# Optimization experiments

Hardware: AMD Instinct MI355X
Metric: run time of the kernel (lower is better)

Reference implementation:

```python
import jax, jax.numpy as jnp
import numpy as np
from jax import lax

B, E, D, N, R, K = 4, 768, 1536, 16, 48, 4
H, W = 16, 16
L = H * W
NDIR = 4


def _perms():
    idx = np.arange(L)
    idx_v = np.arange(L).reshape(H, W).T.reshape(-1)  # column-major (vertical) scan order
    perms = [idx, idx[::-1].copy(), idx_v, idx_v[::-1].copy()]
    invs = [np.argsort(p) for p in perms]
    return [jnp.asarray(p) for p in perms], [jnp.asarray(p) for p in invs]

PERMS, INVS = _perms()


def setup_inputs() -> dict:
    key = jax.random.key(0)
    ks = jax.random.split(key, 10)
    hidden_states = jax.random.normal(ks[0], (B, L, E), jnp.float32)
    in_proj_w = jax.random.normal(ks[1], (2 * D, E), jnp.float32) * 0.02
    out_proj_w = jax.random.normal(ks[2], (E, D), jnp.float32) * 0.02
    conv_w = jax.random.normal(ks[3], (NDIR, D, K), jnp.float32) * 0.1
    conv_b = jax.random.normal(ks[4], (NDIR, D), jnp.float32) * 0.1
    xproj_w = jax.random.normal(ks[5], (NDIR, R + 2 * N, D), jnp.float32) * 0.02
    dt_init_std = R ** -0.5
    dtproj_w = jax.random.uniform(ks[6], (NDIR, D, R), jnp.float32, -dt_init_std, dt_init_std)
    dt = jnp.exp(jax.random.uniform(ks[7], (NDIR, D), jnp.float32)
                 * (np.log(0.1) - np.log(0.001)) + np.log(0.001))
    dt = jnp.clip(dt, 1e-4, None)
    dtproj_b = dt + jnp.log(-jnp.expm1(-dt))  # inverse-softplus init as in the module
    A_log = jnp.broadcast_to(
        jnp.log(jnp.arange(1, N + 1, dtype=jnp.float32))[None, None, :], (NDIR, D, N)).copy()
    D_param = jnp.ones((NDIR, D), jnp.float32)
    return dict(hidden_states=hidden_states, in_proj_w=in_proj_w, out_proj_w=out_proj_w,
                conv_w=conv_w, conv_b=conv_b, xproj_w=xproj_w, dtproj_w=dtproj_w,
                dtproj_b=dtproj_b, A_log=A_log, D_param=D_param)


def _mamba_dir(xz, cw, cb, xw, dtw, dtb, a_log, dpar):
    # xz: (B, 2D, L) in this direction's scan order
    x, z = xz[:, :D], xz[:, D:]
    # causal depthwise conv1d + SiLU (mamba_inner_fn conv path)
    x = lax.conv_general_dilated(x, cw[:, None, :], (1,), [(K - 1, 0)],
                                 feature_group_count=D,
                                 dimension_numbers=('NCH', 'OIH', 'NCH'))
    x = jax.nn.silu(x + cb[None, :, None])
    # x_proj -> dt, B, C
    x_dbl = jnp.einsum('bdl,kd->bkl', x, xw)
    dt, Bm, Cm = x_dbl[:, :R], x_dbl[:, R:R + N], x_dbl[:, R + N:]
    delta = jax.nn.softplus(jnp.einsum('brl,dr->bdl', dt, dtw) + dtb[None, :, None])
    A = -jnp.exp(a_log)                                  # (D, N)
    dA = jnp.exp(jnp.einsum('bdl,dn->lbdn', delta, A))   # (L, B, D, N)
    dBu = jnp.einsum('bdl,bnl,bdl->lbdn', delta, Bm, x)  # delta * B * u

    def step(h, inp):
        da, dbu = inp
        h = da * h + dbu
        return h, h

    h0 = jnp.zeros((x.shape[0], D, N), x.dtype)
    _, hs = lax.scan(step, h0, (dA, dBu))                # (L, B, D, N)
    y = jnp.einsum('lbdn,bnl->bdl', hs, Cm) + dpar[None, :, None] * x
    return y * jax.nn.silu(z)                            # gate, (B, D, L)


def reference(hidden_states, in_proj_w, out_proj_w, conv_w, conv_b,
              xproj_w, dtproj_w, dtproj_b, A_log, D_param):
    xz = jnp.einsum('ble,fe->bfl', hidden_states, in_proj_w)  # (B, 2D, L)
    out = jnp.zeros((hidden_states.shape[0], D, L), hidden_states.dtype)
    for i in range(NDIR):  # fixed small set of structurally distinct scan directions
        xz_i = xz[:, :, PERMS[i]]
        y = _mamba_dir(xz_i, conv_w[i], conv_b[i], xproj_w[i], dtproj_w[i],
                       dtproj_b[i], A_log[i], D_param[i])
        out = out + y[:, :, INVS[i]]  # multi_reverse then sum-fusion
    return jnp.einsum('bdl,ed->ble', out, out_proj_w)
```

## Files before the change

### kernel.cpp

```cpp
#include <hip/hip_runtime.h>
#include <hip/hip_bf16.h>

#define BI   4
#define LI   256
#define EI   768
#define DI   1536
#define NI   16
#define RI   48
#define KI   4
#define NDIRS 4
#define F2D  3072
#define MROWS 1024
#define LOG2E 1.4426950408889634f

typedef float    floatx2 __attribute__((ext_vector_type(2)));
typedef float    floatx4 __attribute__((ext_vector_type(4)));
typedef _Float16 halfx2  __attribute__((ext_vector_type(2)));
typedef _Float16 halfx4  __attribute__((ext_vector_type(4)));
typedef _Float16 halfx8  __attribute__((ext_vector_type(8)));

typedef __attribute__((address_space(3))) unsigned lds_u32;
typedef __attribute__((address_space(1))) const unsigned glb_u32;

__device__ __forceinline__ void load16(const _Float16* g, _Float16* l) {
    __builtin_amdgcn_global_load_lds((glb_u32*)g, (lds_u32*)l, 16, 0, 0);
}

__device__ __forceinline__ int perm_idx(int dir, int j) {
    switch (dir) {
        case 0:  return j;
        case 1:  return 255 - j;
        case 2:  return ((j & 15) << 4) | (j >> 4);
        default: return 255 - (((j & 15) << 4) | (j >> 4));
    }
}

template<int CTRL>
__device__ __forceinline__ float dpp_add(float p) {
    int t = __builtin_amdgcn_update_dpp(0, __builtin_bit_cast(int, p),
                                        CTRL, 0xf, 0xf, true);
    return p + __builtin_bit_cast(float, t);
}
__device__ __forceinline__ float grp8_sum(float p) {
    p = dpp_add<0xB1>(p);
    p = dpp_add<0x4E>(p);
    p = dpp_add<0x141>(p);
    return p;
}

template<int BM, int BN, int WGN, int FM, int FN>
__device__ __forceinline__ void gemm_core(const _Float16* __restrict__ Ah,
                                          const _Float16* __restrict__ Al, int lda,
                                          const _Float16* __restrict__ Bh,
                                          const _Float16* __restrict__ Bl, int ldb,
                                          int nChunks, _Float16* smem,
                                          floatx4 (&acc)[FM][FN]) {
    const int tid = threadIdx.x, lane = tid & 63, wave = tid >> 6;
    const int wave_m = wave / WGN, wave_n = wave % WGN;
    _Float16* sAh = smem;
    _Float16* sAl = smem + BM * 32;
    _Float16* sBh = smem + BM * 64;
    _Float16* sBl = smem + BM * 64 + BN * 32;
    const int rr = lane & 15, koff = (lane >> 4) * 8;
    const int arow = wave_m * FM * 16, brow = wave_n * FN * 16;

    for (int c = 0; c < nChunks; ++c) {
        for (int idx = tid; idx < BM * 4; idx += 256) {
            int r = idx >> 2, s = (idx & 3) * 8;
            load16(Ah + (size_t)r * lda + c * 32 + s, sAh + idx * 8);
            load16(Al + (size_t)r * lda + c * 32 + s, sAl + idx * 8);
        }
        for (int idx = tid; idx < BN * 4; idx += 256) {
            int r = idx >> 2, s = (idx & 3) * 8;
            load16(Bh + (size_t)r * ldb + c * 32 + s, sBh + idx * 8);
            load16(Bl + (size_t)r * ldb + c * 32 + s, sBl + idx * 8);
        }
        asm volatile("s_waitcnt vmcnt(0)" ::: "memory");
        __syncthreads();

        halfx8 ahf[FM], alf[FM], bhf[FN], blf[FN];
        #pragma unroll
        for (int i = 0; i < FM; ++i) {
            ahf[i] = *(const halfx8*)(sAh + (arow + i * 16 + rr) * 32 + koff);
            alf[i] = *(const halfx8*)(sAl + (arow + i * 16 + rr) * 32 + koff);
        }
        #pragma unroll
        for (int j = 0; j < FN; ++j) {
            bhf[j] = *(const halfx8*)(sBh + (brow + j * 16 + rr) * 32 + koff);
            blf[j] = *(const halfx8*)(sBl + (brow + j * 16 + rr) * 32 + koff);
        }
        #pragma unroll
        for (int i = 0; i < FM; ++i)
            #pragma unroll
            for (int j = 0; j < FN; ++j) {
                acc[i][j] = __builtin_amdgcn_mfma_f32_16x16x32_f16(ahf[i], bhf[j], acc[i][j], 0, 0, 0);
                acc[i][j] = __builtin_amdgcn_mfma_f32_16x16x32_f16(ahf[i], blf[j], acc[i][j], 0, 0, 0);
                acc[i][j] = __builtin_amdgcn_mfma_f32_16x16x32_f16(alf[i], bhf[j], acc[i][j], 0, 0, 0);
            }
        __syncthreads();
    }
}

__global__ __launch_bounds__(256) void k_splitall(
        const float* __restrict__ hs,  const float* __restrict__ wip,
        const float* __restrict__ wop, const float* __restrict__ xw,
        const float* __restrict__ dtw,
        _Float16* __restrict__ hsh,  _Float16* __restrict__ hsl,
        _Float16* __restrict__ wiph, _Float16* __restrict__ wipl,
        _Float16* __restrict__ woph, _Float16* __restrict__ wopl,
        _Float16* __restrict__ xwh,  _Float16* __restrict__ xwl,
        _Float16* __restrict__ dtwh, _Float16* __restrict__ dtwl) {
    int i4 = (blockIdx.x * 256 + threadIdx.x) * 4;
    floatx4 v;
    _Float16 *dh, *dl; int off;
    if (i4 < 786432)        { off = i4;           v = *(const floatx4*)(hs + off);  dh = hsh;  dl = hsl;  }
    else if (i4 < 3145728)  { off = i4 - 786432;  v = *(const floatx4*)(wip + off); dh = wiph; dl = wipl; }
    else if (i4 < 4325376)  { off = i4 - 3145728; v = *(const floatx4*)(wop + off); dh = woph; dl = wopl; }
    else if (i4 < 4816896)  { off = i4 - 4325376; v = *(const floatx4*)(xw + off);  dh = xwh;  dl = xwl;  }
    else {
        int t0 = i4 - 4816896;
        int col = t0 & 63, dr = t0 >> 6;
        floatx4 z = {0.f, 0.f, 0.f, 0.f};
        v = (col < 48) ? *(const floatx4*)(dtw + (size_t)dr * 48 + col) : z;
        dh = dtwh; dl = dtwl; off = t0;
    }
    halfx4 hh, hl;
    #pragma unroll
    for (int e = 0; e < 4; ++e) {
        _Float16 h = (_Float16)v[e];
        hh[e] = h; hl[e] = (_Float16)(v[e] - (float)h);
    }
    *(halfx4*)(dh + off) = hh;
    *(halfx4*)(dl + off) = hl;
}

__global__ __launch_bounds__(256) void k_inproj_t(const _Float16* __restrict__ Ah,
                                                  const _Float16* __restrict__ Al,
                                                  const _Float16* __restrict__ Bh,
                                                  const _Float16* __restrict__ Bl,
                                                  float* __restrict__ C) {
    __shared__ _Float16 smem[128 * 64 + 128 * 64];
    int row0 = blockIdx.x * 128, col0 = blockIdx.y * 128, k0 = blockIdx.z * 384;
    float* Cp = C + (size_t)blockIdx.z * MROWS * F2D;
    floatx4 acc[4][4] = {};
    gemm_core<128, 128, 2, 4, 4>(Ah + (size_t)row0 * EI + k0, Al + (size_t)row0 * EI + k0, EI,
                                 Bh + (size_t)col0 * EI + k0, Bl + (size_t)col0 * EI + k0, EI,
                                 12, smem, acc);
    int lane = threadIdx.x & 63, wave = threadIdx.x >> 6;
    int cc = lane & 15, q = lane >> 4;
    int rbase = row0 + (wave >> 1) * 64, cbase = col0 + (wave & 1) * 64;
    #pragma unroll
    for (int i = 0; i < 4; ++i)
        #pragma unroll
        for (int j = 0; j < 4; ++j)
            #pragma unroll
            for (int r = 0; r < 4; ++r)
                Cp[(size_t)(rbase + i * 16 + q * 4 + r) * F2D + cbase + j * 16 + cc] = acc[i][j][r];
}

__global__ __launch_bounds__(256) void k_outproj_t(const _Float16* __restrict__ Ah,
                                                   const _Float16* __restrict__ Al,
                                                   const _Float16* __restrict__ Bh,
                                                   const _Float16* __restrict__ Bl,
                                                   float* __restrict__ C) {
    __shared__ _Float16 smem[192 * 64];
    int row0 = blockIdx.x * 64, col0 = blockIdx.y * 128, k0 = blockIdx.z * 384;
    float* Cp = C + (size_t)blockIdx.z * MROWS * EI;
    floatx4 acc[2][4] = {};
    gemm_core<64, 128, 2, 2, 4>(Ah + (size_t)row0 * DI + k0, Al + (size_t)row0 * DI + k0, DI,
                                Bh + (size_t)col0 * DI + k0, Bl + (size_t)col0 * DI + k0, DI,
                                12, smem, acc);
    int lane = threadIdx.x & 63, wave = threadIdx.x >> 6;
    int cc = lane & 15, q = lane >> 4;
    int rbase = row0 + (wave >> 1) * 32, cbase = col0 + (wave & 1) * 64;
    #pragma unroll
    for (int i = 0; i < 2; ++i)
        #pragma unroll
        for (int j = 0; j < 4; ++j)
            #pragma unroll
            for (int r = 0; r < 4; ++r)
                Cp[(size_t)(rbase + i * 16 + q * 4 + r) * EI + cbase + j * 16 + cc] = acc[i][j][r];
}

__global__ __launch_bounds__(256) void k_osum(const float* __restrict__ oacc,
                                              float* __restrict__ out) {
    int i4 = (blockIdx.x * 256 + threadIdx.x) * 4;
    const size_t S = (size_t)MROWS * EI;
    floatx4 s = *(const floatx4*)(oacc + i4) + *(const floatx4*)(oacc + S + i4) +
                *(const floatx4*)(oacc + 2 * S + i4) + *(const floatx4*)(oacc + 3 * S + i4);
    *(floatx4*)(out + i4) = s;
}

__global__ __launch_bounds__(256) void k_xdbl_t(const _Float16* __restrict__ xh,
                                                const _Float16* __restrict__ xl,
                                                const _Float16* __restrict__ xwh,
                                                const _Float16* __restrict__ xwl,
                                                float* __restrict__ C) {
    __shared__ _Float16 smem[208 * 64];
    int row0 = blockIdx.x * 128, dir = blockIdx.y, k0 = blockIdx.z * 192;
    float* Cp = C + (size_t)blockIdx.z * NDIRS * MROWS * 80;
    floatx4 acc[2][5] = {};
    const size_t abase = ((size_t)dir * MROWS + row0) * DI + k0;
    const size_t bbase = (size_t)dir * 80 * DI + k0;
    gemm_core<128, 80, 1, 2, 5>(xh + abase, xl + abase, DI,
                                xwh + bbase, xwl + bbase, DI, 6, smem, acc);
    int lane = threadIdx.x & 63, wave = threadIdx.x >> 6;
    int cc = lane & 15, q = lane >> 4;
    int rbase = row0 + wave * 32;
    #pragma unroll
    for (int i = 0; i < 2; ++i)
        #pragma unroll
        for (int j = 0; j < 5; ++j)
            #pragma unroll
            for (int r = 0; r < 4; ++r)
                Cp[((size_t)dir * MROWS + rbase + i * 16 + q * 4 + r) * 80 + j * 16 + cc] = acc[i][j][r];
}

__global__ __launch_bounds__(256) void k_xsplit(const float* __restrict__ acc,
                                                _Float16* __restrict__ dtqh,
                                                _Float16* __restrict__ dtql,
                                                float* __restrict__ BCm) {
    const size_t PS = (size_t)NDIRS * MROWS * 80;
    int idx = blockIdx.x * 256 + threadIdx.x;
    int dir = idx / (MROWS * 96);
    int rem = idx - dir * MROWS * 96;
    int row = rem / 96, col = rem - row * 96;
    size_t rbase = (size_t)dir * MROWS + row;
    auto sum8 = [&](int c) {
        size_t o = rbase * 80 + c;
        float s = 0.f;
        #pragma unroll
        for (int kp = 0; kp < 8; ++kp) s += acc[kp * PS + o];
        return s;
    };
    if (col < 64) {
        float v = (col < 48) ? sum8(col) : 0.f;
        _Float16 h = (_Float16)v;
        dtqh[rbase * 64 + col] = h;
        dtql[rbase * 64 + col] = (_Float16)(v - (float)h);
    } else if (col < 80) {
        int n = col - 64;
        BCm[rbase * 32 + n * 2] = sum8(48 + n);
    } else {
        int n = col - 80;
        BCm[rbase * 32 + n * 2 + 1] = sum8(64 + n);
    }
}

__global__ __launch_bounds__(256) void k_delta_t(const _Float16* __restrict__ dtqh,
                                                 const _Float16* __restrict__ dtql,
                                                 const _Float16* __restrict__ dtwh,
                                                 const _Float16* __restrict__ dtwl,
                                                 const float* __restrict__ dtb,
                                                 float* __restrict__ delta) {
    __shared__ _Float16 smem[192 * 64];
    int row0 = blockIdx.x * 64, col0 = blockIdx.y * 128, dir = blockIdx.z;
    floatx4 acc[2][4] = {};
    const size_t abase = ((size_t)dir * MROWS + row0) * 64;
    const size_t bbase = ((size_t)dir * DI + col0) * 64;
    gemm_core<64, 128, 2, 2, 4>(dtqh + abase, dtql + abase, 64,
                                dtwh + bbase, dtwl + bbase, 64, 2, smem, acc);
    int lane = threadIdx.x & 63, wave = threadIdx.x >> 6;
    int cc = lane & 15, q = lane >> 4;
    int rbase = row0 + (wave >> 1) * 32, cbase = col0 + (wave & 1) * 64;
    #pragma unroll
    for (int i = 0; i < 2; ++i)
        #pragma unroll
        for (int j = 0; j < 4; ++j) {
            int col = cbase + j * 16 + cc;
            float bias = dtb[(size_t)dir * DI + col];
            #pragma unroll
            for (int r = 0; r < 4; ++r) {
                float v = acc[i][j][r] + bias;
                float sp = (v > 20.f) ? v : log1pf(__expf(v));
                delta[((size_t)dir * MROWS + rbase + i * 16 + q * 4 + r) * DI + col] = sp;
            }
        }
}

__global__ __launch_bounds__(256) void k_conv(const float* __restrict__ xz,
                                              const float* __restrict__ cw,
                                              const float* __restrict__ cb,
                                              _Float16* __restrict__ xh,
                                              _Float16* __restrict__ xl) {
    const size_t S = (size_t)MROWS * F2D;
    int dir = blockIdx.z, b = blockIdx.y;
    int lchunk = blockIdx.x / 6, dsub = blockIdx.x % 6;
    int d = dsub * 256 + threadIdx.x;
    int base = lchunk * 16;

    const float* w = cw + ((size_t)dir * DI + d) * KI;
    float w0 = w[0], w1 = w[1], w2 = w[2], w3 = w[3];
    float bias = cb[(size_t)dir * DI + d];

    auto ld = [&](int m) -> float {
        if (m < 0) return 0.f;
        int src = perm_idx(dir, m);
        size_t o = ((size_t)b * 256 + src) * F2D + d;
        return xz[o] + xz[S + o];
    };
    float xm3 = ld(base - 3), xm2 = ld(base - 2), xm1 = ld(base - 1);

    #pragma unroll
    for (int j = 0; j < 16; ++j) {
        float cur = ld(base + j);
        float s = bias + w0 * xm3 + w1 * xm2 + w2 * xm1 + w3 * cur;
        xm3 = xm2; xm2 = xm1; xm1 = cur;
        float x = s / (1.f + __expf(-s));
        _Float16 h = (_Float16)x;
        size_t o = ((size_t)dir * MROWS + b * 256 + base + j) * DI + d;
        xh[o] = h;
        xl[o] = (_Float16)(x - (float)h);
    }
}

__global__ __launch_bounds__(256) void k_scan(const float* __restrict__ delta,
                                              const _Float16* __restrict__ xhg,
                                              const _Float16* __restrict__ xlg,
                                              const float* __restrict__ BCm,
                                              const float* __restrict__ A_log,
                                              const float* __restrict__ Dp,
                                              float* __restrict__ ydir) {
    const int dchunk = blockIdx.x, b = blockIdx.y, dir = blockIdx.z;
    const int tid = threadIdx.x;
    const int dslot = tid >> 3;
    const int np = tid & 7;
    const int d0 = dchunk * 32, d = d0 + dslot;

    __shared__ float sdx[2][32][64];
    __shared__ float sbc[2][32][32];
    __shared__ float sY[32][32];

    const float Av0 = -__expf(A_log[((size_t)dir * DI + d) * NI + 2 * np]) * LOG2E;
    const float Av1 = -__expf(A_log[((size_t)dir * DI + d) * NI + 2 * np + 1]) * LOG2E;
    const float Dpar = Dp[(size_t)dir * DI + d];
    float h0 = 0.f, h1 = 0.f;

    const size_t dirrow = (size_t)dir * MROWS;
    const int srow = tid >> 3, sc4 = (tid & 7) * 4;

    floatx4 rdel, rbc;
    halfx4 rxh, rxl;
    auto load_chunk = [&](int j0) {
        int row = b * 256 + j0 + srow;
        size_t o = (dirrow + row) * DI + d0 + sc4;
        rdel = *(const floatx4*)(delta + o);
        rxh  = *(const halfx4*)(xhg + o);
        rxl  = *(const halfx4*)(xlg + o);
        rbc  = *(const floatx4*)(BCm + (dirrow + row) * 32 + sc4);
    };

    load_chunk(0);

    for (int c = 0; c < 8; ++c) {
        const int buf = c & 1;
        #pragma unroll
        for (int e = 0; e < 4; ++e) {
            sdx[buf][srow][(sc4 + e) * 2]     = rdel[e];
            sdx[buf][srow][(sc4 + e) * 2 + 1] = (float)rxh[e] + (float)rxl[e];
        }
        *(floatx4*)&sbc[buf][srow][sc4] = rbc;
        __syncthreads();
        if (c < 7) load_chunk((c + 1) * 32);

        #pragma unroll
        for (int jj = 0; jj < 32; ++jj) {
            floatx2 dx = *(const floatx2*)&sdx[buf][jj][dslot * 2];
            floatx4 bc = *(const floatx4*)&sbc[buf][jj][np * 4];
            float dv = dx[0], xv = dx[1];
            float a0 = __builtin_amdgcn_exp2f(dv * Av0);
            float a1 = __builtin_amdgcn_exp2f(dv * Av1);
            float du = dv * xv;
            h0 = fmaf(a0, h0, du * bc[0]);
            h1 = fmaf(a1, h1, du * bc[2]);
            float p = fmaf(h1, bc[3], h0 * bc[1]);
            p = grp8_sum(p);
            if (np == 0) sY[jj][dslot] = fmaf(Dpar, xv, p);
        }
        __syncthreads();

        {
            int lout = perm_idx(dir, c * 32 + srow);
            floatx4 o = *(const floatx4*)&sY[srow][sc4];
            *(floatx4*)&ydir[(dirrow + (size_t)b * 256 + lout) * DI + d0 + sc4] = o;
        }
    }
}

__global__ __launch_bounds__(256) void k_sum(const float* __restrict__ ydir,
                                             const float* __restrict__ xz,
                                             _Float16* __restrict__ yh,
                                             _Float16* __restrict__ yl) {
    int i4 = (blockIdx.x * 256 + threadIdx.x) * 4;
    const size_t S = (size_t)MROWS * DI;
    const size_t SZ = (size_t)MROWS * F2D;
    int row = i4 / DI, dcol = i4 - row * DI;
    size_t zo = (size_t)row * F2D + DI + dcol;
    floatx4 zv = *(const floatx4*)(xz + zo) + *(const floatx4*)(xz + SZ + zo);
    floatx4 s = *(const floatx4*)(ydir + i4) + *(const floatx4*)(ydir + S + i4) +
                *(const floatx4*)(ydir + 2 * S + i4) + *(const floatx4*)(ydir + 3 * S + i4);
    halfx4 hh, hl;
    #pragma unroll
    for (int e = 0; e < 4; ++e) {
        float g = zv[e] / (1.f + __expf(-zv[e]));
        float v = s[e] * g;
        _Float16 h = (_Float16)v;
        hh[e] = h; hl[e] = (_Float16)(v - (float)h);
    }
    *(halfx4*)(yh + i4) = hh;
    *(halfx4*)(yl + i4) = hl;
}

extern "C" void kernel_launch(void* const* d_in, const int* in_sizes, int n_in,
                              void* d_out, int out_size, void* d_ws, size_t ws_size,
                              hipStream_t stream) {
    const float* hs   = (const float*)d_in[0];
    const float* wip  = (const float*)d_in[1];
    const float* wop  = (const float*)d_in[2];
    const float* cw   = (const float*)d_in[3];
    const float* cb   = (const float*)d_in[4];
    const float* xw   = (const float*)d_in[5];
    const float* dtw  = (const float*)d_in[6];
    const float* dtb  = (const float*)d_in[7];
    const float* alog = (const float*)d_in[8];
    const float* dpar = (const float*)d_in[9];
    float* out = (float*)d_out;

    char* p = (char*)d_ws;
    auto alloc_f32 = [&](size_t n) { float* r = (float*)p; p += n * 4; return r; };
    auto alloc_f16 = [&](size_t n) { _Float16* r = (_Float16*)p; p += n * 2; return r; };

    _Float16* hsh  = alloc_f16(786432);
    _Float16* hsl  = alloc_f16(786432);
    _Float16* wiph = alloc_f16(2359296);
    _Float16* wipl = alloc_f16(2359296);
    _Float16* woph = alloc_f16(1179648);
    _Float16* wopl = alloc_f16(1179648);
    _Float16* xwh  = alloc_f16(491520);
    _Float16* xwl  = alloc_f16(491520);
    _Float16* dtwh = alloc_f16((size_t)NDIRS * DI * 64);
    _Float16* dtwl = alloc_f16((size_t)NDIRS * DI * 64);
    float*    xz   = alloc_f32((size_t)2 * MROWS * F2D);
    _Float16* xh   = alloc_f16((size_t)NDIRS * MROWS * DI);
    _Float16* xl   = alloc_f16((size_t)NDIRS * MROWS * DI);
    _Float16* dtqh = alloc_f16((size_t)NDIRS * MROWS * 64);
    _Float16* dtql = alloc_f16((size_t)NDIRS * MROWS * 64);
    float*    BCm  = alloc_f32((size_t)NDIRS * MROWS * 32);
    float*    delta= alloc_f32((size_t)NDIRS * MROWS * DI);
    float*    ydir = alloc_f32((size_t)NDIRS * MROWS * DI);
    _Float16* yh   = alloc_f16((size_t)MROWS * DI);
    _Float16* yl   = alloc_f16((size_t)MROWS * DI);

    float* xdba = ydir;
    float* oacc = delta;

    k_splitall<<<dim3(5088), 256, 0, stream>>>(hs, wip, wop, xw, dtw,
                                               hsh, hsl, wiph, wipl, woph, wopl,
                                               xwh, xwl, dtwh, dtwl);
    k_inproj_t<<<dim3(8, 24, 2), 256, 0, stream>>>(hsh, hsl, wiph, wipl, xz);
    k_conv    <<<dim3(96, BI, NDIRS), 256, 0, stream>>>(xz, cw, cb, xh, xl);
    k_xdbl_t  <<<dim3(8, NDIRS, 8), 256, 0, stream>>>(xh, xl, xwh, xwl, xdba);
    k_xsplit  <<<dim3(1536), 256, 0, stream>>>(xdba, dtqh, dtql, BCm);
    k_delta_t <<<dim3(16, 12, NDIRS), 256, 0, stream>>>(dtqh, dtql, dtwh, dtwl, dtb, delta);
    k_scan    <<<dim3(DI / 32, BI, NDIRS), 256, 0, stream>>>(delta, xh, xl, BCm,
                                                             alog, dpar, ydir);
    k_sum     <<<dim3(1536), 256, 0, stream>>>(ydir, xz, yh, yl);
    k_outproj_t<<<dim3(16, 6, 4), 256, 0, stream>>>(yh, yl, woph, wopl, oacc);
    k_osum    <<<dim3(768), 256, 0, stream>>>(oacc, out);
}
```

Baseline: 228.5 us.

## Accumulate out-proj split-K with atomics and store delta as f16 hi/lo pair

The out-projection split-K partial buffers and the separate k_osum reduction kernel are removed. The output is now zeroed inside k_splitall and each split-K block atomically adds its partials into the output. Delta is also written as an f16 high/low pair instead of f32, and the scan reconstructs it on load. Traffic per element is unchanged, so the gain comes mainly from one fewer launch and no partial-buffer round trip. The cost is float atomic contention and non-deterministic summation order.

After: 234.2 us. 2.5% more time.

```diff
diff --git a/kernel.cpp b/kernel.cpp
--- a/kernel.cpp
+++ b/kernel.cpp
@@ -109,7 +109,8 @@
         _Float16* __restrict__ wiph, _Float16* __restrict__ wipl,
         _Float16* __restrict__ woph, _Float16* __restrict__ wopl,
         _Float16* __restrict__ xwh,  _Float16* __restrict__ xwl,
-        _Float16* __restrict__ dtwh, _Float16* __restrict__ dtwl) {
+        _Float16* __restrict__ dtwh, _Float16* __restrict__ dtwl,
+        float* __restrict__ outz) {
     int i4 = (blockIdx.x * 256 + threadIdx.x) * 4;
     floatx4 v;
     _Float16 *dh, *dl; int off;
@@ -117,12 +118,17 @@
     else if (i4 < 3145728)  { off = i4 - 786432;  v = *(const floatx4*)(wip + off); dh = wiph; dl = wipl; }
     else if (i4 < 4325376)  { off = i4 - 3145728; v = *(const floatx4*)(wop + off); dh = woph; dl = wopl; }
     else if (i4 < 4816896)  { off = i4 - 4325376; v = *(const floatx4*)(xw + off);  dh = xwh;  dl = xwl;  }
-    else {
+    else if (i4 < 5210112) {
         int t0 = i4 - 4816896;
         int col = t0 & 63, dr = t0 >> 6;
         floatx4 z = {0.f, 0.f, 0.f, 0.f};
         v = (col < 48) ? *(const floatx4*)(dtw + (size_t)dr * 48 + col) : z;
         dh = dtwh; dl = dtwl; off = t0;
+    } else {
+        int t0 = i4 - 5210112;
+        floatx4 z = {0.f, 0.f, 0.f, 0.f};
+        *(floatx4*)(outz + t0) = z;
+        return;
     }
     halfx4 hh, hl;
     #pragma unroll
@@ -165,7 +171,6 @@
                                                    float* __restrict__ C) {
     __shared__ _Float16 smem[192 * 64];
     int row0 = blockIdx.x * 64, col0 = blockIdx.y * 128, k0 = blockIdx.z * 384;
-    float* Cp = C + (size_t)blockIdx.z * MROWS * EI;
     floatx4 acc[2][4] = {};
     gemm_core<64, 128, 2, 2, 4>(Ah + (size_t)row0 * DI + k0, Al + (size_t)row0 * DI + k0, DI,
                                 Bh + (size_t)col0 * DI + k0, Bl + (size_t)col0 * DI + k0, DI,
@@ -179,16 +184,8 @@
         for (int j = 0; j < 4; ++j)
             #pragma unroll
             for (int r = 0; r < 4; ++r)
-                Cp[(size_t)(rbase + i * 16 + q * 4 + r) * EI + cbase + j * 16 + cc] = acc[i][j][r];
-}
-
-__global__ __launch_bounds__(256) void k_osum(const float* __restrict__ oacc,
-                                              float* __restrict__ out) {
-    int i4 = (blockIdx.x * 256 + threadIdx.x) * 4;
-    const size_t S = (size_t)MROWS * EI;
-    floatx4 s = *(const floatx4*)(oacc + i4) + *(const floatx4*)(oacc + S + i4) +
-                *(const floatx4*)(oacc + 2 * S + i4) + *(const floatx4*)(oacc + 3 * S + i4);
-    *(floatx4*)(out + i4) = s;
+                atomicAdd(&C[(size_t)(rbase + i * 16 + q * 4 + r) * EI + cbase + j * 16 + cc],
+                          acc[i][j][r]);
 }
 
 __global__ __launch_bounds__(256) void k_xdbl_t(const _Float16* __restrict__ xh,
@@ -252,7 +249,8 @@
                                                  const _Float16* __restrict__ dtwh,
                                                  const _Float16* __restrict__ dtwl,
                                                  const float* __restrict__ dtb,
-                                                 float* __restrict__ delta) {
+                                                 _Float16* __restrict__ deltah,
+                                                 _Float16* __restrict__ deltal) {
     __shared__ _Float16 smem[192 * 64];
     int row0 = blockIdx.x * 64, col0 = blockIdx.y * 128, dir = blockIdx.z;
     floatx4 acc[2][4] = {};
@@ -273,7 +271,10 @@
             for (int r = 0; r < 4; ++r) {
                 float v = acc[i][j][r] + bias;
                 float sp = (v > 20.f) ? v : log1pf(__expf(v));
-                delta[((size_t)dir * MROWS + rbase + i * 16 + q * 4 + r) * DI + col] = sp;
+                size_t o = ((size_t)dir * MROWS + rbase + i * 16 + q * 4 + r) * DI + col;
+                _Float16 h = (_Float16)sp;
+                deltah[o] = h;
+                deltal[o] = (_Float16)(sp - (float)h);
             }
         }
 }
@@ -314,7 +315,8 @@
     }
 }
 
-__global__ __launch_bounds__(256) void k_scan(const float* __restrict__ delta,
+__global__ __launch_bounds__(256) void k_scan(const _Float16* __restrict__ deltah,
+                                              const _Float16* __restrict__ deltal,
                                               const _Float16* __restrict__ xhg,
                                               const _Float16* __restrict__ xlg,
                                               const float* __restrict__ BCm,
@@ -339,15 +341,16 @@
     const size_t dirrow = (size_t)dir * MROWS;
     const int srow = tid >> 3, sc4 = (tid & 7) * 4;
 
-    floatx4 rdel, rbc;
-    halfx4 rxh, rxl;
+    floatx4 rbc;
+    halfx4 rdh, rdl, rxh, rxl;
     auto load_chunk = [&](int j0) {
         int row = b * 256 + j0 + srow;
         size_t o = (dirrow + row) * DI + d0 + sc4;
-        rdel = *(const floatx4*)(delta + o);
-        rxh  = *(const halfx4*)(xhg + o);
-        rxl  = *(const halfx4*)(xlg + o);
-        rbc  = *(const floatx4*)(BCm + (dirrow + row) * 32 + sc4);
+        rdh = *(const halfx4*)(deltah + o);
+        rdl = *(const halfx4*)(deltal + o);
+        rxh = *(const halfx4*)(xhg + o);
+        rxl = *(const halfx4*)(xlg + o);
+        rbc = *(const floatx4*)(BCm + (dirrow + row) * 32 + sc4);
     };
 
     load_chunk(0);
@@ -356,7 +359,7 @@
         const int buf = c & 1;
         #pragma unroll
         for (int e = 0; e < 4; ++e) {
-            sdx[buf][srow][(sc4 + e) * 2]     = rdel[e];
+            sdx[buf][srow][(sc4 + e) * 2]     = (float)rdh[e] + (float)rdl[e];
             sdx[buf][srow][(sc4 + e) * 2 + 1] = (float)rxh[e] + (float)rxl[e];
         }
         *(floatx4*)&sbc[buf][srow][sc4] = rbc;
@@ -446,25 +449,25 @@
     _Float16* dtqh = alloc_f16((size_t)NDIRS * MROWS * 64);
     _Float16* dtql = alloc_f16((size_t)NDIRS * MROWS * 64);
     float*    BCm  = alloc_f32((size_t)NDIRS * MROWS * 32);
-    float*    delta= alloc_f32((size_t)NDIRS * MROWS * DI);
+    _Float16* deltah = alloc_f16((size_t)NDIRS * MROWS * DI);
+    _Float16* deltal = alloc_f16((size_t)NDIRS * MROWS * DI);
     float*    ydir = alloc_f32((size_t)NDIRS * MROWS * DI);
     _Float16* yh   = alloc_f16((size_t)MROWS * DI);
     _Float16* yl   = alloc_f16((size_t)MROWS * DI);
 
     float* xdba = ydir;
-    float* oacc = delta;
-
-    k_splitall<<<dim3(5088), 256, 0, stream>>>(hs, wip, wop, xw, dtw,
+
+    k_splitall<<<dim3(5856), 256, 0, stream>>>(hs, wip, wop, xw, dtw,
                                                hsh, hsl, wiph, wipl, woph, wopl,
-                                               xwh, xwl, dtwh, dtwl);
+                                               xwh, xwl, dtwh, dtwl, out);
     k_inproj_t<<<dim3(8, 24, 2), 256, 0, stream>>>(hsh, hsl, wiph, wipl, xz);
     k_conv    <<<dim3(96, BI, NDIRS), 256, 0, stream>>>(xz, cw, cb, xh, xl);
     k_xdbl_t  <<<dim3(8, NDIRS, 8), 256, 0, stream>>>(xh, xl, xwh, xwl, xdba);
     k_xsplit  <<<dim3(1536), 256, 0, stream>>>(xdba, dtqh, dtql, BCm);
-    k_delta_t <<<dim3(16, 12, NDIRS), 256, 0, stream>>>(dtqh, dtql, dtwh, dtwl, dtb, delta);
-    k_scan    <<<dim3(DI / 32, BI, NDIRS), 256, 0, stream>>>(delta, xh, xl, BCm,
+    k_delta_t <<<dim3(16, 12, NDIRS), 256, 0, stream>>>(dtqh, dtql, dtwh, dtwl, dtb,
+                                                        deltah, deltal);
+    k_scan    <<<dim3(DI / 32, BI, NDIRS), 256, 0, stream>>>(deltah, deltal, xh, xl, BCm,
                                                              alog, dpar, ydir);
     k_sum     <<<dim3(1536), 256, 0, stream>>>(ydir, xz, yh, yl);
-    k_outproj_t<<<dim3(16, 6, 4), 256, 0, stream>>>(yh, yl, woph, wopl, oacc);
-    k_osum    <<<dim3(768), 256, 0, stream>>>(oacc, out);
-}
+    k_outproj_t<<<dim3(16, 6, 4), 256, 0, stream>>>(yh, yl, woph, wopl, out);
+}
```
